# Performance work log

Hardware: AMD Instinct MI355X
Metric: run time of the kernel (lower is better)

Reference implementation:

```python
import jax, jax.numpy as jnp
import numpy as np

NH = 8       # num_heads
EDIM = 256   # embedding_dim (also per-head dim in this module)
BS, SQL = 4, 1024


def setup_inputs() -> dict:
    key = jax.random.key(0)
    ks = jax.random.split(key, 5)
    scale_in = 1.0 / np.sqrt(EDIM)
    scale_out = 1.0 / np.sqrt(NH * EDIM)
    return {
        "x": jax.random.normal(ks[0], (BS, SQL, EDIM), dtype=jnp.float32),
        "w_attn": jax.random.normal(ks[1], (NH * 3 * EDIM, EDIM), dtype=jnp.float32) * scale_in,
        "b_attn": jax.random.normal(ks[2], (NH * 3 * EDIM,), dtype=jnp.float32) * scale_in,
        "w_out": jax.random.normal(ks[3], (EDIM, NH * EDIM), dtype=jnp.float32) * scale_out,
        "b_out": jax.random.normal(ks[4], (EDIM,), dtype=jnp.float32) * scale_out,
    }


def reference(x, w_attn, b_attn, w_out, b_out):
    bs, sql, edim = x.shape
    nh = NH
    # projections: (bs, sql, nh*3*edim); split into Q, K, V chunks of nh*edim
    proj = x @ w_attn.T + b_attn
    q, k, v = jnp.split(proj, 3, axis=-1)
    # Faithful to torch: raw view (bs, sql, nh*edim) -> (bs, nh, sql, edim),
    # a reinterpretation of memory, NOT a transpose.
    q = q.reshape(bs, nh, sql, edim)
    k = k.reshape(bs, nh, sql, edim)
    v = v.reshape(bs, nh, sql, edim)
    # scaled dot-product scores: (bs, nh, sql, sql)
    scores = jnp.einsum("bhqd,bhkd->bhqk", q, k) / jnp.sqrt(jnp.float32(edim))
    # causal mask: -inf strictly above the diagonal (equivalent to adding triu(-inf, 1))
    causal = jnp.tril(jnp.ones((sql, sql), dtype=bool))
    scores = jnp.where(causal, scores, -jnp.inf)
    attn = jax.nn.softmax(scores, axis=-1)
    out = jnp.einsum("bhqk,bhkd->bhqd", attn, v)
    # Faithful raw view back: (bs, nh, sql, edim) -> (bs, sql, nh*edim)
    out = out.reshape(bs, sql, nh * edim)
    return out @ w_out.T + b_out
```

## Files before the change

### kernel.cpp

```cpp
#include <hip/hip_runtime.h>

#define SQL  1024
#define EDIM 256
#define NHD  8
#define NKV  (NHD * 3 * EDIM)
#define MROWS (4 * SQL)

typedef short bf16x8 __attribute__((ext_vector_type(8)));
typedef float f32x4 __attribute__((ext_vector_type(4)));

__device__ __forceinline__ unsigned short f2bf(float f) {
  unsigned u = __float_as_uint(f);
  u += 0x7fff + ((u >> 16) & 1);
  return (unsigned short)(u >> 16);
}

__device__ __forceinline__ void g2lds16(const void* g, void* l) {
  __builtin_amdgcn_global_load_lds(
      (const __attribute__((address_space(1))) unsigned int*)g,
      (__attribute__((address_space(3))) unsigned int*)l, 16, 0, 0);
}

__device__ __forceinline__ void storev(float* p, float v) { *p = v; }
__device__ __forceinline__ void storev(unsigned short* p, float v) { *p = f2bf(v); }

__global__ __launch_bounds__(256) void cast3_bf16(
    const float* __restrict__ s0, unsigned short* __restrict__ d0, int n0,
    const float* __restrict__ s1, unsigned short* __restrict__ d1, int n1,
    const float* __restrict__ s2, unsigned short* __restrict__ d2, int n2) {
  int i = blockIdx.x * 256 + threadIdx.x;
  const float* s; unsigned short* d;
  if (i < n0) { s = s0; d = d0; }
  else if (i < n0 + n1) { i -= n0; s = s1; d = d1; }
  else { i -= n0 + n1; if (i >= n2) return; s = s2; d = d2; }
  float4 a = ((const float4*)s)[2 * i];
  float4 b = ((const float4*)s)[2 * i + 1];
  union { unsigned short u[8]; ulonglong2 v; } t;
  t.u[0] = f2bf(a.x); t.u[1] = f2bf(a.y); t.u[2] = f2bf(a.z); t.u[3] = f2bf(a.w);
  t.u[4] = f2bf(b.x); t.u[5] = f2bf(b.y); t.u[6] = f2bf(b.z); t.u[7] = f2bf(b.w);
  ((ulonglong2*)d)[i] = t.v;
}

template <int BM, int BN, typename OutT>
__global__ __launch_bounds__(256) void gemm_mfma(
    const unsigned short* __restrict__ A, const unsigned short* __restrict__ B,
    const float* __restrict__ bias, OutT* __restrict__ C,
    int M, int N, int K) {
  constexpr int TM = BM / 32, TN = BN / 32;
  __shared__ __align__(16) unsigned short As[2][BM * 32];
  __shared__ __align__(16) unsigned short Bs[2][BN * 32];
  const int tid = threadIdx.x;
  const int wave = tid >> 6, lane = tid & 63;
  const int quad = lane >> 4, l16 = lane & 15;
  const int wm = (wave >> 1) * (BM / 2), wn = (wave & 1) * (BN / 2);
  const int m0 = blockIdx.x * BM, n0 = blockIdx.y * BN;
  const int sw = (l16 >> 1) & 3;

  f32x4 acc[TM][TN];
  #pragma unroll
  for (int i = 0; i < TM; i++)
    #pragma unroll
    for (int j = 0; j < TN; j++) acc[i][j] = {0.f, 0.f, 0.f, 0.f};

  auto stage = [&](int k0, int bb) {
    #pragma unroll
    for (int it = 0; it < BM / 64; it++) {
      int flat = it * 256 + tid;
      int row = flat >> 2;
      int cg = (flat & 3) ^ ((row >> 1) & 3);
      g2lds16(A + (size_t)(m0 + row) * K + k0 + cg * 8, &As[bb][flat * 8]);
    }
    #pragma unroll
    for (int it = 0; it < BN / 64; it++) {
      int flat = it * 256 + tid;
      int row = flat >> 2;
      int cg = (flat & 3) ^ ((row >> 1) & 3);
      g2lds16(B + (size_t)(n0 + row) * K + k0 + cg * 8, &Bs[bb][flat * 8]);
    }
  };

  stage(0, 0);
  __syncthreads();
  for (int k0 = 0; k0 < K; k0 += 32) {
    const int bb = (k0 >> 5) & 1;
    if (k0 + 32 < K) stage(k0 + 32, bb ^ 1);
    bf16x8 af[TM], bf[TN];
    #pragma unroll
    for (int i = 0; i < TM; i++)
      af[i] = *(const bf16x8*)&As[bb][(wm + i * 16 + l16) * 32 + (quad ^ sw) * 8];
    #pragma unroll
    for (int j = 0; j < TN; j++)
      bf[j] = *(const bf16x8*)&Bs[bb][(wn + j * 16 + l16) * 32 + (quad ^ sw) * 8];
    #pragma unroll
    for (int i = 0; i < TM; i++)
      #pragma unroll
      for (int j = 0; j < TN; j++)
        acc[i][j] = __builtin_amdgcn_mfma_f32_16x16x32_bf16(af[i], bf[j], acc[i][j], 0, 0, 0);
    __syncthreads();
  }

  #pragma unroll
  for (int i = 0; i < TM; i++) {
    #pragma unroll
    for (int r = 0; r < 4; r++) {
      int m = m0 + wm + i * 16 + quad * 4 + r;
      #pragma unroll
      for (int j = 0; j < TN; j++) {
        int n = n0 + wn + j * 16 + l16;
        storev(&C[(size_t)m * N + n], acc[i][j][r] + bias[n]);
      }
    }
  }
}

__global__ __launch_bounds__(256) void transpose_v(
    const unsigned short* __restrict__ proj, unsigned short* __restrict__ vt) {
  __shared__ unsigned short T[64][66];
  const int tid = threadIdx.x;
  const int s0 = blockIdx.x * 64, d0 = blockIdx.y * 64, bh = blockIdx.z;
  const int b = bh >> 3, h = bh & 7;
  #pragma unroll
  for (int it = 0; it < 2; it++) {
    int c = it * 256 + tid;
    int sr = c >> 3, k8 = (c & 7) * 8;
    int s = s0 + sr;
    const unsigned short* src = proj + (size_t)(b * SQL + h * 128 + (s >> 3)) * NKV
                                + 2 * 2048 + (s & 7) * 256 + d0 + k8;
    *(ulonglong2*)&T[sr][k8] = *(const ulonglong2*)src;
  }
  __syncthreads();
  #pragma unroll
  for (int it = 0; it < 2; it++) {
    int c = it * 256 + tid;
    int dr = c >> 3, s8 = (c & 7) * 8;
    unsigned short tmp[8];
    #pragma unroll
    for (int j = 0; j < 8; j++) tmp[j] = T[s8 + j][dr];
    const int d = d0 + dr;
    const int t = (s0 + s8) >> 5;
    const int j = (s8 >> 3) & 3;
    const int cj = j ^ ((d >> 1) & 3);
    unsigned short* dst = vt + (((size_t)bh * 32 + t) * 1024 + d * 4 + cj) * 8;
    *(ulonglong2*)dst = *(ulonglong2*)tmp;
  }
}

__global__ __launch_bounds__(512, 2) void attn_mfma(
    const unsigned short* __restrict__ proj,
    const unsigned short* __restrict__ vt,
    unsigned short* __restrict__ oflat) {
  __shared__ __align__(16) unsigned short lds[70656];
  __shared__ float lsumX[4][16];
  unsigned short* Ps = lds + 65536;

  const int tid = threadIdx.x;
  const int wave = tid >> 6, lane = tid & 63;
  const int quad = lane >> 4, l16 = lane & 15;
  const int qs = wave >> 1;
  const int p  = wave & 1;
  const int slot = blockIdx.x & 255, round = blockIdx.x >> 8;
  const int bh = slot & 31;
  const int jj = slot >> 5;
  const int qt = round ? jj : 15 - jj;
  const int b = bh >> 3, h = bh & 7;
  const int q0 = qt * 64;

  auto stagepair = [&](int pr, int bb) {
    unsigned short* B = lds + bb * 32768;
    #pragma unroll
    for (int it = 0; it < 4; it++) {
      int c = it * 512 + tid;
      int r = c >> 5, ch = (c & 31) ^ (r & 7);
      int s = pr * 64 + r;
      g2lds16(proj + (size_t)(b * SQL + h * 128 + (s >> 3)) * NKV + 2048 + (s & 7) * 256 + ch * 8,
              B + c * 8);
    }
    const unsigned short* vsrc = vt + ((size_t)bh * 32 + pr * 2) * 8192;
    #pragma unroll
    for (int it = 0; it < 4; it++) {
      int c = it * 512 + tid;
      g2lds16(vsrc + c * 8, B + 16384 + c * 8);
    }
  };

  stagepair(0, 0);
  #pragma unroll
  for (int it = 0; it < 4; it++) {
    int c = it * 512 + tid;
    int r = c >> 5, ch = (c & 31) ^ (r & 7);
    int s = q0 + r;
    g2lds16(proj + (size_t)(b * SQL + h * 128 + (s >> 3)) * NKV + (s & 7) * 256 + ch * 8,
            lds + 32768 + c * 8);
  }
  __syncthreads();
  bf16x8 aq[8];
  const int qrow = qs * 16 + l16;
  #pragma unroll
  for (int kk = 0; kk < 8; kk++)
    aq[kk] = *(const bf16x8*)&lds[32768 + qrow * 256 + ((kk * 4 + quad) ^ (qrow & 7)) * 8];
  __syncthreads();

  f32x4 o[16];
  #pragma unroll
  for (int t = 0; t < 16; t++) o[t] = {0.f, 0.f, 0.f, 0.f};
  float l_r[4] = {0.f, 0.f, 0.f, 0.f};

  const int np = qt + 1;
  for (int pr = 0; pr < np; pr++) {
    const int bb = pr & 1;
    if (pr + 1 < np) stagepair(pr + 1, bb ^ 1);
    unsigned short* B = lds + bb * 32768;
    const unsigned short* KsB = B + p * 8192;
    const unsigned short* VtB = B + 16384 + p * 8192;
    const int my_kt = 2 * pr + p;
    const bool live = (my_kt * 32 <= q0 + qs * 16 + 15);

    if (live) {
      f32x4 s0 = {0.f, 0.f, 0.f, 0.f}, s1 = {0.f, 0.f, 0.f, 0.f};
      #pragma unroll
      for (int kk = 0; kk < 8; kk++) {
        int ch = (kk * 4 + quad) ^ (l16 & 7);
        bf16x8 b0 = *(const bf16x8*)&KsB[l16 * 256 + ch * 8];
        bf16x8 b1 = *(const bf16x8*)&KsB[(16 + l16) * 256 + ch * 8];
        s0 = __builtin_amdgcn_mfma_f32_16x16x32_bf16(aq[kk], b0, s0, 0, 0, 0);
        s1 = __builtin_amdgcn_mfma_f32_16x16x32_bf16(aq[kk], b1, s1, 0, 0, 0);
      }

      const int kg0 = my_kt * 32 + l16, kg1 = kg0 + 16;
      unsigned short* PsW = Ps + wave * 640;
      #pragma unroll
      for (int r = 0; r < 4; r++) {
        int qg = q0 + qs * 16 + quad * 4 + r;
        float p0 = (kg0 <= qg) ? exp2f(s0[r] * 0.09016844f) : 0.f;
        float p1 = (kg1 <= qg) ? exp2f(s1[r] * 0.09016844f) : 0.f;
        l_r[r] += p0 + p1;
        PsW[(quad * 4 + r) * 40 + l16]      = f2bf(p0);
        PsW[(quad * 4 + r) * 40 + 16 + l16] = f2bf(p1);
      }

      bf16x8 ap = *(const bf16x8*)&PsW[l16 * 40 + quad * 8];
      #pragma unroll
      for (int tl = 0; tl < 16; tl++) {
        const int d = tl * 16 + l16;
        bf16x8 bv = *(const bf16x8*)&VtB[d * 32 + (quad ^ ((d >> 1) & 3)) * 8];
        o[tl] = __builtin_amdgcn_mfma_f32_16x16x32_bf16(ap, bv, o[tl], 0, 0, 0);
      }
    }
    __syncthreads();
  }

  float lr[4];
  #pragma unroll
  for (int r = 0; r < 4; r++) {
    float l = l_r[r];
    #pragma unroll
    for (int off = 1; off < 16; off <<= 1) l += __shfl_xor(l, off);
    lr[r] = l;
  }
  if (p == 1) {
    f32x4* ob = (f32x4*)lds;
    #pragma unroll
    for (int t = 0; t < 16; t++) ob[(qs * 16 + t) * 64 + lane] = o[t];
    if (l16 == 0) {
      #pragma unroll
      for (int r = 0; r < 4; r++) lsumX[qs][quad * 4 + r] = lr[r];
    }
  }
  __syncthreads();
  if (p == 0) {
    const f32x4* ob = (const f32x4*)lds;
    #pragma unroll
    for (int t = 0; t < 16; t++) o[t] += ob[(qs * 16 + t) * 64 + lane];
    float inv[4];
    #pragma unroll
    for (int r = 0; r < 4; r++) inv[r] = 1.0f / (lr[r] + lsumX[qs][quad * 4 + r]);
    #pragma unroll
    for (int r = 0; r < 4; r++) {
      int s = q0 + qs * 16 + quad * 4 + r;
      unsigned short* dst = oflat + (size_t)(b * SQL + h * 128 + (s >> 3)) * 2048 + (s & 7) * 256;
      #pragma unroll
      for (int t = 0; t < 16; t++)
        dst[t * 16 + l16] = f2bf(o[t][r] * inv[r]);
    }
  }
}

extern "C" void kernel_launch(void* const* d_in, const int* in_sizes, int n_in,
                              void* d_out, int out_size, void* d_ws, size_t ws_size,
                              hipStream_t stream) {
  const float* x      = (const float*)d_in[0];
  const float* w_attn = (const float*)d_in[1];
  const float* b_attn = (const float*)d_in[2];
  const float* w_out  = (const float*)d_in[3];
  const float* b_out  = (const float*)d_in[4];
  float* out = (float*)d_out;

  char* p = (char*)d_ws;
  unsigned short* proj = (unsigned short*)p;  p += (size_t)MROWS * NKV * 2;
  unsigned short* obf  = (unsigned short*)p;  p += (size_t)MROWS * 2048 * 2;
  unsigned short* vtb  = (unsigned short*)p;  p += (size_t)32 * EDIM * SQL * 2;
  unsigned short* xb   = (unsigned short*)p;  p += (size_t)MROWS * EDIM * 2;
  unsigned short* wb   = (unsigned short*)p;  p += (size_t)NKV * EDIM * 2;
  unsigned short* wob  = (unsigned short*)p;

  const int n0 = MROWS * EDIM / 8;
  const int n1 = NKV * EDIM / 8;
  const int n2 = EDIM * 2048 / 8;
  cast3_bf16<<<(n0 + n1 + n2) / 256, 256, 0, stream>>>(x, xb, n0, w_attn, wb, n1,
                                                       w_out, wob, n2);

  gemm_mfma<128, 128, unsigned short><<<dim3(MROWS / 128, NKV / 128), 256, 0, stream>>>(
      xb, wb, b_attn, proj, MROWS, NKV, EDIM);
  transpose_v<<<dim3(SQL / 64, EDIM / 64, 32), 256, 0, stream>>>(proj, vtb);
  attn_mfma<<<512, 512, 0, stream>>>(proj, vtb, obf);
  gemm_mfma<64, 64, float><<<dim3(MROWS / 64, EDIM / 64), 256, 0, stream>>>(
      obf, wob, b_out, out, MROWS, EDIM, NHD * EDIM);
}
```

Before: 173.9 us.

## Halve attention K/V tile to 32 keys and switch PV to 16x16x16 MFMA

The attention kernel now double-buffers single 32-key K/V tiles instead of 64-key pairs, which roughly halves the LDS footprint so more blocks can be resident per CU. The launch bound rises to 4 blocks per CU. Each wave pair splits a tile into 16-key halves and uses 16x16x16 bf16 MFMA for P·V, with the V transpose kernel rewritten to a matching 4-element-chunk layout. The cost is twice as many loop iterations and barriers, smaller and less efficient MFMAs, and possible register spills under the tighter launch bound.

```diff
diff --git a/kernel.cpp b/kernel.cpp
--- a/kernel.cpp
+++ b/kernel.cpp
@@ -7,7 +7,24 @@
 #define MROWS (4 * SQL)
 
 typedef short bf16x8 __attribute__((ext_vector_type(8)));
+typedef short bf16x4 __attribute__((ext_vector_type(4)));
 typedef float f32x4 __attribute__((ext_vector_type(4)));
+
+#if defined(__has_builtin)
+#if __has_builtin(__builtin_amdgcn_mfma_f32_16x16x16bf16_1k)
+#define MFMA16(a, b, c) __builtin_amdgcn_mfma_f32_16x16x16bf16_1k(a, b, c, 0, 0, 0)
+#define HAVE_MFMA16 1
+#elif __has_builtin(__builtin_amdgcn_mfma_f32_16x16x16_bf16)
+#define MFMA16(a, b, c) __builtin_amdgcn_mfma_f32_16x16x16_bf16(a, b, c, 0, 0, 0)
+#define HAVE_MFMA16 1
+#else
+#define HAVE_MFMA16 0
+#endif
+#else
+#define HAVE_MFMA16 0
+#endif
+
+constexpr int PSTR = HAVE_MFMA16 ? 20 : 24;
 
 __device__ __forceinline__ unsigned short f2bf(float f) {
   unsigned u = __float_as_uint(f);
@@ -122,42 +139,47 @@
   #pragma unroll
   for (int it = 0; it < 2; it++) {
     int c = it * 256 + tid;
-    int sr = c >> 3, k8 = (c & 7) * 8;
+    int sr = c >> 3, d8 = (c & 7) * 8;
     int s = s0 + sr;
     const unsigned short* src = proj + (size_t)(b * SQL + h * 128 + (s >> 3)) * NKV
-                                + 2 * 2048 + (s & 7) * 256 + d0 + k8;
-    *(ulonglong2*)&T[sr][k8] = *(const ulonglong2*)src;
+                                + 2 * 2048 + (s & 7) * 256 + d0 + d8;
+    *(ulonglong2*)&T[sr][d8] = *(const ulonglong2*)src;
   }
   __syncthreads();
   #pragma unroll
   for (int it = 0; it < 2; it++) {
     int c = it * 256 + tid;
-    int dr = c >> 3, s8 = (c & 7) * 8;
+    int dr = c & 63, sg = c >> 6;
     unsigned short tmp[8];
     #pragma unroll
-    for (int j = 0; j < 8; j++) tmp[j] = T[s8 + j][dr];
+    for (int j = 0; j < 8; j++) tmp[j] = T[sg * 8 + j][dr];
     const int d = d0 + dr;
-    const int t = (s0 + s8) >> 5;
-    const int j = (s8 >> 3) & 3;
-    const int cj = j ^ ((d >> 1) & 3);
-    unsigned short* dst = vt + (((size_t)bh * 32 + t) * 1024 + d * 4 + cj) * 8;
-    *(ulonglong2*)dst = *(ulonglong2*)tmp;
-  }
-}
-
-__global__ __launch_bounds__(512, 2) void attn_mfma(
+    const int t = (s0 >> 5) + (sg >> 2);
+    const int c4 = (sg & 3) * 2;
+    unsigned short* base = vt + (((size_t)(bh * 32 + t) * 8 + c4) * 256 + d) * 4;
+    uint2 w0, w1;
+    w0.x = (unsigned)tmp[0] | ((unsigned)tmp[1] << 16);
+    w0.y = (unsigned)tmp[2] | ((unsigned)tmp[3] << 16);
+    w1.x = (unsigned)tmp[4] | ((unsigned)tmp[5] << 16);
+    w1.y = (unsigned)tmp[6] | ((unsigned)tmp[7] << 16);
+    *(uint2*)base          = w0;
+    *(uint2*)(base + 1024) = w1;
+  }
+}
+
+__global__ __launch_bounds__(512, 4) void attn_mfma(
     const unsigned short* __restrict__ proj,
     const unsigned short* __restrict__ vt,
     unsigned short* __restrict__ oflat) {
-  __shared__ __align__(16) unsigned short lds[70656];
+  __shared__ __align__(16) unsigned short lds[32768 + 8 * 16 * PSTR];
   __shared__ float lsumX[4][16];
-  unsigned short* Ps = lds + 65536;
+  unsigned short* Ps = lds + 32768;
 
   const int tid = threadIdx.x;
   const int wave = tid >> 6, lane = tid & 63;
   const int quad = lane >> 4, l16 = lane & 15;
   const int qs = wave >> 1;
-  const int p  = wave & 1;
+  const int kh = wave & 1;
   const int slot = blockIdx.x & 255, round = blockIdx.x >> 8;
   const int bh = slot & 31;
   const int jj = slot >> 5;
@@ -165,39 +187,39 @@
   const int b = bh >> 3, h = bh & 7;
   const int q0 = qt * 64;
 
-  auto stagepair = [&](int pr, int bb) {
-    unsigned short* B = lds + bb * 32768;
-    #pragma unroll
-    for (int it = 0; it < 4; it++) {
+  auto stage = [&](int kt, int bb) {
+    unsigned short* B = lds + bb * 16384;
+    #pragma unroll
+    for (int it = 0; it < 2; it++) {
       int c = it * 512 + tid;
       int r = c >> 5, ch = (c & 31) ^ (r & 7);
-      int s = pr * 64 + r;
+      int s = kt * 32 + r;
       g2lds16(proj + (size_t)(b * SQL + h * 128 + (s >> 3)) * NKV + 2048 + (s & 7) * 256 + ch * 8,
               B + c * 8);
     }
-    const unsigned short* vsrc = vt + ((size_t)bh * 32 + pr * 2) * 8192;
-    #pragma unroll
-    for (int it = 0; it < 4; it++) {
+    const unsigned short* vsrc = vt + ((size_t)bh * 32 + kt) * 8192;
+    #pragma unroll
+    for (int it = 0; it < 2; it++) {
       int c = it * 512 + tid;
-      g2lds16(vsrc + c * 8, B + 16384 + c * 8);
+      g2lds16(vsrc + c * 8, B + 8192 + c * 8);
     }
   };
 
-  stagepair(0, 0);
+  stage(0, 0);
   #pragma unroll
   for (int it = 0; it < 4; it++) {
     int c = it * 512 + tid;
     int r = c >> 5, ch = (c & 31) ^ (r & 7);
     int s = q0 + r;
     g2lds16(proj + (size_t)(b * SQL + h * 128 + (s >> 3)) * NKV + (s & 7) * 256 + ch * 8,
-            lds + 32768 + c * 8);
+            lds + 16384 + c * 8);
   }
   __syncthreads();
   bf16x8 aq[8];
   const int qrow = qs * 16 + l16;
   #pragma unroll
   for (int kk = 0; kk < 8; kk++)
-    aq[kk] = *(const bf16x8*)&lds[32768 + qrow * 256 + ((kk * 4 + quad) ^ (qrow & 7)) * 8];
+    aq[kk] = *(const bf16x8*)&lds[16384 + qrow * 256 + ((kk * 4 + quad) ^ (qrow & 7)) * 8];
   __syncthreads();
 
   f32x4 o[16];
@@ -205,46 +227,55 @@
   for (int t = 0; t < 16; t++) o[t] = {0.f, 0.f, 0.f, 0.f};
   float l_r[4] = {0.f, 0.f, 0.f, 0.f};
 
-  const int np = qt + 1;
-  for (int pr = 0; pr < np; pr++) {
-    const int bb = pr & 1;
-    if (pr + 1 < np) stagepair(pr + 1, bb ^ 1);
-    unsigned short* B = lds + bb * 32768;
-    const unsigned short* KsB = B + p * 8192;
-    const unsigned short* VtB = B + 16384 + p * 8192;
-    const int my_kt = 2 * pr + p;
-    const bool live = (my_kt * 32 <= q0 + qs * 16 + 15);
+  const int nkt = 2 * qt + 2;
+  for (int kt = 0; kt < nkt; kt++) {
+    const int bb = kt & 1;
+    if (kt + 1 < nkt) stage(kt + 1, bb ^ 1);
+    const unsigned short* KsB = lds + bb * 16384;
+    const unsigned short* VtB = KsB + 8192;
+    const bool live = (kt * 32 + kh * 16 <= q0 + qs * 16 + 15);
 
     if (live) {
-      f32x4 s0 = {0.f, 0.f, 0.f, 0.f}, s1 = {0.f, 0.f, 0.f, 0.f};
+      f32x4 s0 = {0.f, 0.f, 0.f, 0.f};
+      const int krow = kh * 16 + l16;
       #pragma unroll
       for (int kk = 0; kk < 8; kk++) {
-        int ch = (kk * 4 + quad) ^ (l16 & 7);
-        bf16x8 b0 = *(const bf16x8*)&KsB[l16 * 256 + ch * 8];
-        bf16x8 b1 = *(const bf16x8*)&KsB[(16 + l16) * 256 + ch * 8];
-        s0 = __builtin_amdgcn_mfma_f32_16x16x32_bf16(aq[kk], b0, s0, 0, 0, 0);
-        s1 = __builtin_amdgcn_mfma_f32_16x16x32_bf16(aq[kk], b1, s1, 0, 0, 0);
-      }
-
-      const int kg0 = my_kt * 32 + l16, kg1 = kg0 + 16;
-      unsigned short* PsW = Ps + wave * 640;
+        bf16x8 bk = *(const bf16x8*)&KsB[krow * 256 + ((kk * 4 + quad) ^ (l16 & 7)) * 8];
+        s0 = __builtin_amdgcn_mfma_f32_16x16x32_bf16(aq[kk], bk, s0, 0, 0, 0);
+      }
+
+      const int kg = kt * 32 + kh * 16 + l16;
+      unsigned short* PsW = Ps + wave * 16 * PSTR;
       #pragma unroll
       for (int r = 0; r < 4; r++) {
         int qg = q0 + qs * 16 + quad * 4 + r;
-        float p0 = (kg0 <= qg) ? exp2f(s0[r] * 0.09016844f) : 0.f;
-        float p1 = (kg1 <= qg) ? exp2f(s1[r] * 0.09016844f) : 0.f;
-        l_r[r] += p0 + p1;
-        PsW[(quad * 4 + r) * 40 + l16]      = f2bf(p0);
-        PsW[(quad * 4 + r) * 40 + 16 + l16] = f2bf(p1);
-      }
-
-      bf16x8 ap = *(const bf16x8*)&PsW[l16 * 40 + quad * 8];
+        float p0 = (kg <= qg) ? exp2f(s0[r] * 0.09016844f) : 0.f;
+        l_r[r] += p0;
+        PsW[(quad * 4 + r) * PSTR + l16] = f2bf(p0);
+      }
+
+#if HAVE_MFMA16
+      bf16x4 ap = *(const bf16x4*)&PsW[l16 * PSTR + quad * 4];
       #pragma unroll
       for (int tl = 0; tl < 16; tl++) {
         const int d = tl * 16 + l16;
-        bf16x8 bv = *(const bf16x8*)&VtB[d * 32 + (quad ^ ((d >> 1) & 3)) * 8];
-        o[tl] = __builtin_amdgcn_mfma_f32_16x16x32_bf16(ap, bv, o[tl], 0, 0, 0);
-      }
+        bf16x4 bv = *(const bf16x4*)&VtB[((kh * 4 + quad) * 256 + d) * 4];
+        o[tl] = MFMA16(ap, bv, o[tl]);
+      }
+#else
+      bf16x8 ap8;
+      if (quad < 2) ap8 = *(const bf16x8*)&PsW[l16 * PSTR + quad * 8];
+      else          ap8 = bf16x8{0, 0, 0, 0, 0, 0, 0, 0};
+      const int c4a = kh * 4 + (quad & 1) * 2;
+      #pragma unroll
+      for (int tl = 0; tl < 16; tl++) {
+        const int d = tl * 16 + l16;
+        union { bf16x8 v8; bf16x4 v4[2]; } bvu;
+        bvu.v4[0] = *(const bf16x4*)&VtB[(c4a * 256 + d) * 4];
+        bvu.v4[1] = *(const bf16x4*)&VtB[((c4a + 1) * 256 + d) * 4];
+        o[tl] = __builtin_amdgcn_mfma_f32_16x16x32_bf16(ap8, bvu.v8, o[tl], 0, 0, 0);
+      }
+#endif
     }
     __syncthreads();
   }
@@ -257,7 +288,7 @@
     for (int off = 1; off < 16; off <<= 1) l += __shfl_xor(l, off);
     lr[r] = l;
   }
-  if (p == 1) {
+  if (kh == 1) {
     f32x4* ob = (f32x4*)lds;
     #pragma unroll
     for (int t = 0; t < 16; t++) ob[(qs * 16 + t) * 64 + lane] = o[t];
@@ -267,7 +298,7 @@
     }
   }
   __syncthreads();
-  if (p == 0) {
+  if (kh == 0) {
     const f32x4* ob = (const f32x4*)lds;
     #pragma unroll
     for (int t = 0; t < 16; t++) o[t] += ob[(qs * 16 + t) * 64 + lane];
```

Measured after the change: 206.6 us. +18.8%, slower.
